# Optimization experiments

Hardware: AMD Instinct MI355X
Metric: run time of the kernel (lower is better)

Reference implementation:

```python
import jax, jax.numpy as jnp
import numpy as np

T = 3
B, N, F = 8, 256, 32
E_DIM = 8
HID = 32
IN_DIM = 2 * (F + 1) + E_DIM  # 74


def setup_inputs() -> dict:
    key = jax.random.key(0)
    ks = jax.random.split(key, 10)
    h = jax.random.normal(ks[0], (B, N, F), dtype=jnp.float32)
    e = jax.random.uniform(ks[1], (B, N, N, E_DIM), dtype=jnp.float32)
    q = jax.random.normal(ks[2], (B, N, 1), dtype=jnp.float32)
    mask = jnp.ones((B, N), dtype=jnp.float32)
    s1 = 1.0 / np.sqrt(IN_DIM)
    s2 = 1.0 / np.sqrt(HID)
    W1 = jax.random.normal(ks[3], (T, IN_DIM, HID), dtype=jnp.float32) * s1
    b1 = jnp.zeros((T, HID), dtype=jnp.float32)
    W2 = jax.random.normal(ks[4], (T, HID, HID), dtype=jnp.float32) * s2
    b2 = jnp.zeros((T, HID), dtype=jnp.float32)
    W3 = jax.random.normal(ks[5], (T, HID, 1), dtype=jnp.float32) * s2
    b3 = jnp.zeros((T, 1), dtype=jnp.float32)
    return {"h": h, "e": e, "q": q, "mask": mask,
            "W1": W1, "b1": b1, "W2": W2, "b2": b2, "W3": W3, "b3": b3}


def reference(h, e, q, mask, W1, b1, W2, b2, W3, b3):
    tol = jnp.float32(1e-8)
    clip = jnp.clip(e, tol, 1e5)
    largest_e = jnp.max(clip, axis=-1)          # [B,N,N]
    is_near = (largest_e != tol).astype(h.dtype)
    m = mask.astype(h.dtype)
    exp_mask = m[:, :, None] * m[:, None, :]    # [B,N,N]
    natom = e.shape[1]

    def mlp(x, t):
        x = jax.nn.relu(jnp.matmul(x, W1[t]) + b1[t])
        x = jax.nn.relu(jnp.matmul(x, W2[t]) + b2[t])
        return (jnp.matmul(x, W3[t]) + b3[t])[..., 0]  # [B,N,N]

    for t in range(T):
        inp = jnp.concatenate([h, q], axis=-1)  # [B,N,F+1]
        d = inp.shape[-1]
        inp_i = jnp.broadcast_to(inp[:, :, None, :], (inp.shape[0], natom, natom, d))
        inp_j = jnp.broadcast_to(inp[:, None, :, :], (inp.shape[0], natom, natom, d))
        inp_ij = jnp.concatenate([inp_i, inp_j, e], axis=-1)  # [B,N,N,IN_DIM]
        inp_ji = jnp.concatenate([inp_j, inp_i, e], axis=-1)
        elec_ij = mlp(inp_ij, t)
        elec_ji = mlp(inp_ji, t)
        antisym = 0.5 * (elec_ij - elec_ji) * exp_mask * is_near
        q = q + jnp.sum(antisym, axis=2)[..., None]
    return q
```

## Files before the change

kernel.cpp:

```cpp
#include <hip/hip_runtime.h>
#include <hip/hip_bf16.h>


typedef __attribute__((ext_vector_type(8))) short short8;
typedef __attribute__((ext_vector_type(4))) short short4v;
typedef __attribute__((ext_vector_type(4))) float f32x4;
union U4S8 { uint4 u; short8 s; };
union U2S4 { uint2 u; short4v s; };
#define F4(p) (*(const float4*)(p))

#if defined(__HIP_DEVICE_COMPILE__)
# if __has_builtin(__builtin_amdgcn_mfma_f32_16x16x16bf16_1k)
#  define MFMA16(a,b,c) __builtin_amdgcn_mfma_f32_16x16x16bf16_1k(a,b,c,0,0,0)
# elif __has_builtin(__builtin_amdgcn_mfma_f32_16x16x16_bf16)
#  define MFMA16(a,b,c) __builtin_amdgcn_mfma_f32_16x16x16_bf16(a,b,c,0,0,0)
# else
#  error "no 16x16x16 bf16 MFMA builtin on this target"
# endif
#else
# define MFMA16(a,b,c) (f32x4{0.f,0.f,0.f,0.f})
#endif

__device__ __forceinline__ unsigned pkbf2(float lo, float hi) {
    unsigned a = __bfloat16_as_ushort(__float2bfloat16(lo));
    unsigned b = __bfloat16_as_ushort(__float2bfloat16(hi));
    return a | (b << 16);
}
__device__ __forceinline__ float bf2f(unsigned short u) {
    return __uint_as_float(((unsigned)u) << 16);
}

__global__ __launch_bounds__(256) void epn_pre(
    const float* __restrict__ h, const float* __restrict__ W1,
    const float* __restrict__ b1, const float* __restrict__ W2,
    unsigned short* __restrict__ basePbf, unsigned short* __restrict__ baseQbf,
    uint2* __restrict__ W2T16, uint4* __restrict__ WA)
{
    const int t  = blockIdx.x >> 8;
    const int lg = (blockIdx.x & 255) * 256 + threadIdx.x;
    const float* W1t = W1 + t*2368;
    if (lg < 256) {
        int f = lg >> 6, lane = lg & 63;
        int kh = f >> 1, nt = f & 1;
        int sl = lane >> 4, l15 = lane & 15;
        int k0 = kh*16 + sl*4, n = nt*16 + l15;
        const float* W2t = W2 + t*1024;
        W2T16[t*256 + lg] = make_uint2(
            pkbf2(W2t[k0*32 + n],     W2t[(k0+1)*32 + n]),
            pkbf2(W2t[(k0+2)*32 + n], W2t[(k0+3)*32 + n]));
    } else if (lg < 384) {
        int g2 = lg - 256;
        int kt = g2 >> 6, lane = g2 & 63;
        int l15 = lane & 15, sl = lane >> 4;
        float v[8];
        #pragma unroll
        for (int p = 0; p < 8; ++p) {
            int d = sl*8 + p;
            v[p] = (d < 8) ? W1t[(66+d)*32 + kt*16 + l15]
                           : ((kt*16 + l15 == d - 8) ? 1.0f : 0.0f);
        }
        WA[t*128 + g2] = make_uint4(pkbf2(v[0],v[1]), pkbf2(v[2],v[3]),
                                    pkbf2(v[4],v[5]), pkbf2(v[6],v[7]));
    }
    const int node = lg >> 5, k = lg & 31;
    const float* hn = h + node*32;
    float p = b1[t*32 + k], qq = 0.f;
    #pragma unroll
    for (int f = 0; f < 32; ++f) {
        float hv = hn[f];
        p  += hv * W1t[f*32 + k];
        qq += hv * W1t[(33+f)*32 + k];
    }
    basePbf[t*65536 + lg] = __bfloat16_as_ushort(__float2bfloat16(p));
    baseQbf[t*65536 + lg] = __bfloat16_as_ushort(__float2bfloat16(qq));
}

__global__ __launch_bounds__(256, 4) void epn_main(
    const float* __restrict__ e, const float* __restrict__ mask,
    const uint4* __restrict__ bP4, const uint4* __restrict__ bQ4,
    const float* __restrict__ qrowP, const float* __restrict__ qrowQ,
    const uint2* __restrict__ W2T16, const uint4* __restrict__ WA,
    const float* __restrict__ b2, const float* __restrict__ W3,
    const float* __restrict__ q_src, float* __restrict__ q_dst)
{
    __shared__ uint4 sx[9][256];
    __shared__ float mnL[256];
    __shared__ float red[4];

    const int orig = blockIdx.x;
    const int bi = (orig & 7) * 256 + (orig >> 3);
    const int b = bi >> 8;
    const int tid = threadIdx.x, j = tid;
    const int lane = tid & 63, w = tid >> 6;
    const int l15 = lane & 15, sl = lane >> 4;

    float qj = q_src[b*256 + j];
    unsigned qpk = __bfloat16_as_ushort(__float2bfloat16(qj));
    const float* ejp = e + ((size_t)bi*256 + j)*8;
    float4 e0 = F4(ejp), e1 = F4(ejp + 4);
    float mx = fmaxf(fmaxf(fmaxf(e0.x,e0.y),fmaxf(e0.z,e0.w)),
                     fmaxf(fmaxf(e1.x,e1.y),fmaxf(e1.z,e1.w)));
    float nearf = (fminf(fmaxf(mx, 1e-8f), 1e5f) != 1e-8f) ? 1.f : 0.f;
    mnL[j] = mask[bi] * mask[b*256 + j] * nearf;
    sx[0][j] = make_uint4(pkbf2(e0.x,e0.y), pkbf2(e0.z,e0.w),
                          pkbf2(e1.x,e1.y), pkbf2(e1.z,e1.w));
    {
        const uint4* bq = bQ4 + (size_t)(b*256 + j)*4;
        const uint4* bp = bP4 + (size_t)(b*256 + j)*4;
        sx[1][j]=bq[0]; sx[2][j]=bq[1]; sx[3][j]=bq[2]; sx[4][j]=bq[3];
        sx[5][j]=bp[0]; sx[6][j]=bp[1]; sx[7][j]=bp[2]; sx[8][j]=bp[3];
    }

    U4S8 wa00, wa01, wa1;
    wa00.u = WA[lane];
    wa01.u = WA[64 + lane];
    wa1.u  = make_uint4(0u,0u,0u,0u);
    if (sl == 0 && l15 >= 8) {
        int p = l15 - 8;
        unsigned v = 0x3F80u << ((p & 1) * 16);
        wa1.u.x = ((p>>1)==0)?v:0u;  wa1.u.y = ((p>>1)==1)?v:0u;
        wa1.u.z = ((p>>1)==2)?v:0u;  wa1.u.w = ((p>>1)==3)?v:0u;
    }
    unsigned aqQ0 = 0, aqQ1 = 0, aqP0 = 0, aqP1 = 0;
    if (sl == 0) {
        aqQ0 = __bfloat16_as_ushort(__float2bfloat16(qrowQ[l15]));
        aqQ1 = __bfloat16_as_ushort(__float2bfloat16(qrowQ[16 + l15]));
        aqP0 = __bfloat16_as_ushort(__float2bfloat16(qrowP[l15]));
        aqP1 = __bfloat16_as_ushort(__float2bfloat16(qrowP[16 + l15]));
    }
    float qi = q_src[bi];
    const unsigned short* bPi = (const unsigned short*)bP4 + (size_t)bi*32;
    const unsigned short* bQi = (const unsigned short*)bQ4 + (size_t)bi*32;
    f32x4 ckP0, ckP1, ckQ0, ckQ1;
    #pragma unroll
    for (int r = 0; r < 4; ++r) {
        int k0 = sl*4 + r, k1 = 16 + sl*4 + r;
        ckP0[r] = bf2f(bPi[k0]) + qi * qrowP[k0];
        ckP1[r] = bf2f(bPi[k1]) + qi * qrowP[k1];
        ckQ0[r] = bf2f(bQi[k0]) + qi * qrowQ[k0];
        ckQ1[r] = bf2f(bQi[k1]) + qi * qrowQ[k1];
    }
    U2S4 bu00, bu10, bu01, bu11;
    bu00.u = W2T16[0*64 + lane];
    bu01.u = W2T16[1*64 + lane];
    bu10.u = W2T16[2*64 + lane];
    bu11.u = W2T16[3*64 + lane];
    float b2v0 = b2[l15], b2v1 = b2[l15+16];
    float w3v0 = W3[l15], w3v1 = W3[l15+16];
    const int slot0_d0 = (sl == 0) ? 0 : sl;
    const int slot0_d1 = (sl == 0) ? 0 : 4 + sl;

    float tot = 0.f;
    __builtin_amdgcn_s_setprio(1);
    #pragma unroll
    for (int rt = 0; rt < 4; ++rt) {
        const int rl  = rt*16 + l15;
        const int row = w*64 + rl;
        unsigned qr = __shfl(qpk, rl);
        U4S8 bc2; bc2.u = make_uint4((sl == 0) ? (qr & 0xFFFFu) : 0u, 0u, 0u, 0u);
        float pA[4], pB[4];
        #pragma unroll
        for (int dir = 0; dir < 2; ++dir) {
            U4S8 bc0, bc1, aq0, aq1;
            bc0.u = sx[dir ? slot0_d1 : slot0_d0][row];
            bc1.u = sx[dir ? 8 : 4][row];
            aq0.u = make_uint4(dir ? aqP0 : aqQ0, 0u, 0u, 0u);
            aq1.u = make_uint4(dir ? aqP1 : aqQ1, 0u, 0u, 0u);
            f32x4 c0v = dir ? ckQ0 : ckP0;
            f32x4 c1v = dir ? ckQ1 : ckP1;
            f32x4 dk0 = __builtin_amdgcn_mfma_f32_16x16x32_bf16(wa00.s, bc0.s, c0v, 0,0,0);
            dk0 = __builtin_amdgcn_mfma_f32_16x16x32_bf16(aq0.s, bc2.s, dk0, 0,0,0);
            f32x4 dk1 = __builtin_amdgcn_mfma_f32_16x16x32_bf16(wa01.s, bc0.s, c1v, 0,0,0);
            dk1 = __builtin_amdgcn_mfma_f32_16x16x32_bf16(wa1.s,  bc1.s, dk1, 0,0,0);
            dk1 = __builtin_amdgcn_mfma_f32_16x16x32_bf16(aq1.s,  bc2.s, dk1, 0,0,0);
            U2S4 a0, a1;
            a0.u = make_uint2(pkbf2(fmaxf(dk0[0],0.f), fmaxf(dk0[1],0.f)),
                              pkbf2(fmaxf(dk0[2],0.f), fmaxf(dk0[3],0.f)));
            a1.u = make_uint2(pkbf2(fmaxf(dk1[0],0.f), fmaxf(dk1[1],0.f)),
                              pkbf2(fmaxf(dk1[2],0.f), fmaxf(dk1[3],0.f)));
            f32x4 z = {0.f, 0.f, 0.f, 0.f};
            f32x4 d0 = MFMA16(a0.s, bu00.s, z);
            d0 = MFMA16(a1.s, bu10.s, d0);
            f32x4 d1 = MFMA16(a0.s, bu01.s, z);
            d1 = MFMA16(a1.s, bu11.s, d1);
            float* pp = dir ? pB : pA;
            pp[0] = fmaxf(d0[0]+b2v0,0.f)*w3v0 + fmaxf(d1[0]+b2v1,0.f)*w3v1;
            pp[1] = fmaxf(d0[1]+b2v0,0.f)*w3v0 + fmaxf(d1[1]+b2v1,0.f)*w3v1;
            pp[2] = fmaxf(d0[2]+b2v0,0.f)*w3v0 + fmaxf(d1[2]+b2v1,0.f)*w3v1;
            pp[3] = fmaxf(d0[3]+b2v0,0.f)*w3v0 + fmaxf(d1[3]+b2v1,0.f)*w3v1;
        }
        float4 mr = *(const float4*)&mnL[w*64 + rt*16 + sl*4];
        tot += mr.x*(pA[0]-pB[0]) + mr.y*(pA[1]-pB[1])
             + mr.z*(pA[2]-pB[2]) + mr.w*(pA[3]-pB[3]);
    }
    __builtin_amdgcn_s_setprio(0);
    #pragma unroll
    for (int off = 32; off > 0; off >>= 1) tot += __shfl_down(tot, off);
    if (lane == 0) red[w] = tot;
    __syncthreads();
    if (tid == 0)
        q_dst[bi] = q_src[bi] + 0.5f * (red[0] + red[1] + red[2] + red[3]);
}

extern "C" void kernel_launch(void* const* d_in, const int* in_sizes, int n_in,
                              void* d_out, int out_size, void* d_ws, size_t ws_size,
                              hipStream_t stream) {
    (void)in_sizes; (void)n_in; (void)out_size; (void)ws_size;
    const float* h    = (const float*)d_in[0];
    const float* e    = (const float*)d_in[1];
    const float* q    = (const float*)d_in[2];
    const float* mask = (const float*)d_in[3];
    const float* W1   = (const float*)d_in[4];
    const float* b1   = (const float*)d_in[5];
    const float* W2   = (const float*)d_in[6];
    const float* b2   = (const float*)d_in[7];
    const float* W3   = (const float*)d_in[8];

    char* ws = (char*)d_ws;
    unsigned short* basePbf = (unsigned short*)ws;
    unsigned short* baseQbf = (unsigned short*)(ws + 393216);
    float* qA   = (float*)(ws + 786432);
    float* qB   = (float*)(ws + 794624);
    uint2* W2T16 = (uint2*)(ws + 802816);
    uint4* WA    = (uint4*)(ws + 808960);

    epn_pre<<<768, 256, 0, stream>>>(h, W1, b1, W2, basePbf, baseQbf, W2T16, WA);

    const float* qsrc = q;
    for (int t = 0; t < 3; ++t) {
        float* qdst = (t == 2) ? (float*)d_out : (t == 0 ? qA : qB);
        epn_main<<<2048, 256, 0, stream>>>(
            e, mask,
            (const uint4*)(basePbf + t*65536), (const uint4*)(baseQbf + t*65536),
            W1 + t*2368 + 32*32, W1 + t*2368 + 65*32,
            W2T16 + t*256, WA + t*128,
            b2 + t*32, W3 + t*32, qsrc, qdst);
        qsrc = qdst;
    }
}
```

Measured before the change: 52.53 us.

## Process four output rows per block, one wave per row, reusing staged j-data

Each block now covers four i-rows, with each wave sweeping all 256 j for its own row, instead of four waves splitting one row. The j-side P/Q basis vectors staged in shared memory are loaded once per block and reused across the four rows. This cuts redundant global and LDS staging traffic and removes the cross-wave shared reduction and its barrier. The grid shrinks from 2048 to 512 blocks and the launch bound drops to 2 blocks per SM, which lowers available parallelism and latency hiding. Shared memory per block grows to hold four rows of e and mask data.

Result: no change. 53.25 us (+1.4%).

```diff
diff --git a/kernel.cpp b/kernel.cpp
--- a/kernel.cpp
+++ b/kernel.cpp
@@ -75,7 +75,7 @@
     baseQbf[t*65536 + lg] = __bfloat16_as_ushort(__float2bfloat16(qq));
 }
 
-__global__ __launch_bounds__(256, 4) void epn_main(
+__global__ __launch_bounds__(256, 2) void epn_main(
     const float* __restrict__ e, const float* __restrict__ mask,
     const uint4* __restrict__ bP4, const uint4* __restrict__ bQ4,
     const float* __restrict__ qrowP, const float* __restrict__ qrowQ,
@@ -83,32 +83,39 @@
     const float* __restrict__ b2, const float* __restrict__ W3,
     const float* __restrict__ q_src, float* __restrict__ q_dst)
 {
-    __shared__ uint4 sx[9][256];
-    __shared__ float mnL[256];
-    __shared__ float red[4];
+    __shared__ uint4 sxJ[8][256];
+    __shared__ uint4 se[4][256];
+    __shared__ float mnL[4][256];
+    __shared__ unsigned short qL[256];
 
     const int orig = blockIdx.x;
-    const int bi = (orig & 7) * 256 + (orig >> 3);
-    const int b = bi >> 8;
+    const int swz  = (orig & 7) * 64 + (orig >> 3);
+    const int b    = swz >> 6;
+    const int bi0  = b*256 + (swz & 63)*4;
     const int tid = threadIdx.x, j = tid;
     const int lane = tid & 63, w = tid >> 6;
     const int l15 = lane & 15, sl = lane >> 4;
-
-    float qj = q_src[b*256 + j];
-    unsigned qpk = __bfloat16_as_ushort(__float2bfloat16(qj));
-    const float* ejp = e + ((size_t)bi*256 + j)*8;
-    float4 e0 = F4(ejp), e1 = F4(ejp + 4);
-    float mx = fmaxf(fmaxf(fmaxf(e0.x,e0.y),fmaxf(e0.z,e0.w)),
-                     fmaxf(fmaxf(e1.x,e1.y),fmaxf(e1.z,e1.w)));
-    float nearf = (fminf(fmaxf(mx, 1e-8f), 1e5f) != 1e-8f) ? 1.f : 0.f;
-    mnL[j] = mask[bi] * mask[b*256 + j] * nearf;
-    sx[0][j] = make_uint4(pkbf2(e0.x,e0.y), pkbf2(e0.z,e0.w),
-                          pkbf2(e1.x,e1.y), pkbf2(e1.z,e1.w));
+    const int bi  = bi0 + w;
+
     {
         const uint4* bq = bQ4 + (size_t)(b*256 + j)*4;
         const uint4* bp = bP4 + (size_t)(b*256 + j)*4;
-        sx[1][j]=bq[0]; sx[2][j]=bq[1]; sx[3][j]=bq[2]; sx[4][j]=bq[3];
-        sx[5][j]=bp[0]; sx[6][j]=bp[1]; sx[7][j]=bp[2]; sx[8][j]=bp[3];
+        sxJ[0][j]=bq[0]; sxJ[1][j]=bq[1]; sxJ[2][j]=bq[2]; sxJ[3][j]=bq[3];
+        sxJ[4][j]=bp[0]; sxJ[5][j]=bp[1]; sxJ[6][j]=bp[2]; sxJ[7][j]=bp[3];
+    }
+    float qj = q_src[b*256 + j];
+    qL[j] = __bfloat16_as_ushort(__float2bfloat16(qj));
+    float maskj = mask[b*256 + j];
+    #pragma unroll
+    for (int p = 0; p < 4; ++p) {
+        const float* ejp = e + ((size_t)(bi0 + p)*256 + j)*8;
+        float4 e0 = F4(ejp), e1 = F4(ejp + 4);
+        float mx = fmaxf(fmaxf(fmaxf(e0.x,e0.y),fmaxf(e0.z,e0.w)),
+                         fmaxf(fmaxf(e1.x,e1.y),fmaxf(e1.z,e1.w)));
+        float nearf = (fminf(fmaxf(mx, 1e-8f), 1e5f) != 1e-8f) ? 1.f : 0.f;
+        mnL[p][j] = mask[bi0 + p] * maskj * nearf;
+        se[p][j] = make_uint4(pkbf2(e0.x,e0.y), pkbf2(e0.z,e0.w),
+                              pkbf2(e1.x,e1.y), pkbf2(e1.z,e1.w));
     }
 
     U4S8 wa00, wa01, wa1;
@@ -147,23 +154,23 @@
     bu11.u = W2T16[3*64 + lane];
     float b2v0 = b2[l15], b2v1 = b2[l15+16];
     float w3v0 = W3[l15], w3v1 = W3[l15+16];
-    const int slot0_d0 = (sl == 0) ? 0 : sl;
-    const int slot0_d1 = (sl == 0) ? 0 : 4 + sl;
+
+    __syncthreads();
 
     float tot = 0.f;
     __builtin_amdgcn_s_setprio(1);
-    #pragma unroll
-    for (int rt = 0; rt < 4; ++rt) {
-        const int rl  = rt*16 + l15;
-        const int row = w*64 + rl;
-        unsigned qr = __shfl(qpk, rl);
-        U4S8 bc2; bc2.u = make_uint4((sl == 0) ? (qr & 0xFFFFu) : 0u, 0u, 0u, 0u);
+    #pragma unroll 4
+    for (int rt = 0; rt < 16; ++rt) {
+        const int row = rt*16 + l15;
+        unsigned qpk = (sl == 0) ? (unsigned)qL[row] : 0u;
+        U4S8 bc2; bc2.u = make_uint4(qpk, 0u, 0u, 0u);
         float pA[4], pB[4];
         #pragma unroll
         for (int dir = 0; dir < 2; ++dir) {
             U4S8 bc0, bc1, aq0, aq1;
-            bc0.u = sx[dir ? slot0_d1 : slot0_d0][row];
-            bc1.u = sx[dir ? 8 : 4][row];
+            bc0.u = (sl == 0) ? se[w][row]
+                              : (dir ? sxJ[3 + sl][row] : sxJ[sl - 1][row]);
+            bc1.u = dir ? sxJ[7][row] : sxJ[3][row];
             aq0.u = make_uint4(dir ? aqP0 : aqQ0, 0u, 0u, 0u);
             aq1.u = make_uint4(dir ? aqP1 : aqQ1, 0u, 0u, 0u);
             f32x4 c0v = dir ? ckQ0 : ckP0;
@@ -189,17 +196,16 @@
             pp[2] = fmaxf(d0[2]+b2v0,0.f)*w3v0 + fmaxf(d1[2]+b2v1,0.f)*w3v1;
             pp[3] = fmaxf(d0[3]+b2v0,0.f)*w3v0 + fmaxf(d1[3]+b2v1,0.f)*w3v1;
         }
-        float4 mr = *(const float4*)&mnL[w*64 + rt*16 + sl*4];
+        float4 mr = *(const float4*)&mnL[w][rt*16 + sl*4];
         tot += mr.x*(pA[0]-pB[0]) + mr.y*(pA[1]-pB[1])
              + mr.z*(pA[2]-pB[2]) + mr.w*(pA[3]-pB[3]);
     }
     __builtin_amdgcn_s_setprio(0);
+
     #pragma unroll
     for (int off = 32; off > 0; off >>= 1) tot += __shfl_down(tot, off);
-    if (lane == 0) red[w] = tot;
-    __syncthreads();
-    if (tid == 0)
-        q_dst[bi] = q_src[bi] + 0.5f * (red[0] + red[1] + red[2] + red[3]);
+    if (lane == 0)
+        q_dst[bi] = q_src[bi] + 0.5f * tot;
 }
 
 extern "C" void kernel_launch(void* const* d_in, const int* in_sizes, int n_in,
@@ -229,7 +235,7 @@
     const float* qsrc = q;
     for (int t = 0; t < 3; ++t) {
         float* qdst = (t == 2) ? (float*)d_out : (t == 0 ? qA : qB);
-        epn_main<<<2048, 256, 0, stream>>>(
+        epn_main<<<512, 256, 0, stream>>>(
             e, mask,
             (const uint4*)(basePbf + t*65536), (const uint4*)(baseQbf + t*65536),
             W1 + t*2368 + 32*32, W1 + t*2368 + 65*32,
```
